# Optimization experiments

Hardware: AMD Instinct MI355X
Metric: run time of the kernel (lower is better)

## Reference

```python
import jax, jax.numpy as jnp
import numpy as np

B, H, KVH, D, CACHE = 16, 32, 8, 128, 4096


def _rope(x, cos, sin):
    # x: [B, S, Hx, D]; cos/sin: [B, S, 1, D//2] -- complex rotation on (even, odd) pairs
    xe, xo = x[..., ::2], x[..., 1::2]
    re = xe * cos - xo * sin
    im = xe * sin + xo * cos
    return jnp.stack([re, im], axis=-1).reshape(x.shape)


def setup_inputs() -> dict:
    key = jax.random.key(0)
    ks = jax.random.split(key, 8)
    xq = jax.random.normal(ks[0], (B, 1, H, D), jnp.float32)
    xk = jax.random.normal(ks[1], (B, 1, KVH, D), jnp.float32)
    xv = jax.random.normal(ks[2], (B, 1, KVH, D), jnp.float32)
    input_pos = jax.random.randint(ks[3], (B,), 1024, CACHE - 1, dtype=jnp.int32)
    inv_freq = 1.0 / (10000.0 ** (jnp.arange(0, D, 2, dtype=jnp.float32) / D))
    ang = input_pos.astype(jnp.float32)[:, None] * inv_freq[None, :]  # [B, D/2]
    freqs_cos = jnp.cos(ang)[:, None, :]  # [B, 1, D/2]
    freqs_sin = jnp.sin(ang)[:, None, :]
    cache_k = jax.random.randint(ks[4], (B, KVH, CACHE, D), -127, 128, dtype=jnp.int32)
    cache_v = jax.random.randint(ks[5], (B, KVH, CACHE, D), -127, 128, dtype=jnp.int32)
    k_scaler = jax.random.uniform(ks[6], (B, KVH, CACHE), jnp.float32, minval=0.005, maxval=0.05)
    v_scaler = jax.random.uniform(ks[7], (B, KVH, CACHE), jnp.float32, minval=0.005, maxval=0.05)
    return dict(xq=xq, xk=xk, xv=xv, freqs_cos=freqs_cos, freqs_sin=freqs_sin,
                k_scaler=k_scaler, v_scaler=v_scaler, cache_k=cache_k, cache_v=cache_v,
                input_pos=input_pos)


def reference(xq, xk, xv, freqs_cos, freqs_sin, k_scaler, v_scaler, cache_k, cache_v, input_pos):
    B_, S_, H_, D_ = xq.shape
    KVH_ = xk.shape[2]
    n_rep = H_ // KVH_
    cos, sin = freqs_cos[:, :, None, :], freqs_sin[:, :, None, :]
    q = _rope(xq, cos, sin)
    k = _rope(xk, cos, sin)
    # new decode token, [B, KVH, D]
    k_new = jnp.transpose(k, (0, 2, 1, 3))[:, :, 0, :]
    v_new = jnp.transpose(xv, (0, 2, 1, 3))[:, :, 0, :]
    # per-token, per-kv-head int8 quantization of the new K/V
    k_s = jnp.max(jnp.abs(k_new), axis=-1, keepdims=True) / 127.0 + 1e-8
    v_s = jnp.max(jnp.abs(v_new), axis=-1, keepdims=True) / 127.0 + 1e-8
    k_q = jnp.clip(jnp.round(k_new / k_s), -127, 127).astype(cache_k.dtype)
    v_q = jnp.clip(jnp.round(v_new / v_s), -127, 127).astype(cache_v.dtype)
    b_idx = jnp.arange(B_)
    cache_k = cache_k.at[b_idx, :, input_pos].set(k_q)
    cache_v = cache_v.at[b_idx, :, input_pos].set(v_q)
    k_scaler = k_scaler.at[b_idx, :, input_pos].set(k_s[..., 0])
    v_scaler = v_scaler.at[b_idx, :, input_pos].set(v_s[..., 0])
    # GQA: group query heads per kv head instead of materializing repeat_kv
    qg = jnp.transpose(q, (0, 2, 1, 3)).reshape(B_, KVH_, n_rep, D_)  # S_ == 1
    scores = jnp.einsum('bkrd,bksd->bkrs', qg, cache_k.astype(jnp.float32))
    scores = scores / jnp.sqrt(jnp.float32(D_)) * k_scaler[:, :, None, :]  # inline K dequant
    S_cache = cache_k.shape[2]
    mask = jnp.where(jnp.arange(S_cache)[None, :] <= input_pos[:, None], 0.0, -1e30)
    probs = jax.nn.softmax(scores + mask[:, None, None, :].astype(scores.dtype), axis=-1)
    out = jnp.einsum('bkrs,bksd->bkrd', probs * v_scaler[:, :, None, :], cache_v.astype(jnp.float32))
    return out.reshape(B_, H_, 1, D_)
```

## Files before the change

### kernel.cpp

```cpp
#include <hip/hip_runtime.h>
#include <hip/hip_bf16.h>
#include <cstdint>
#include <cstddef>

#define BATCH 16
#define HQ 32
#define KVHN 8
#define NREP 4
#define DIM 128
#define CACHE_LEN 4096
#define STATE_POS 128
#define NSTATE (CACHE_LEN / STATE_POS)

__global__ __launch_bounds__(64) void attn_partial(
    const float* __restrict__ xq,
    const float* __restrict__ fcos,
    const float* __restrict__ fsin,
    const float* __restrict__ k_scaler,
    const float* __restrict__ v_scaler,
    const int*   __restrict__ cache_k,
    const int*   __restrict__ cache_v,
    const int*   __restrict__ input_pos,
    float* __restrict__ ws_acc,
    float* __restrict__ ws_ml)
{
    const int state = blockIdx.x;
    const int kvh   = blockIdx.y;
    const int b     = blockIdx.z;
    const int pos   = input_pos[b];
    const int start = state * STATE_POS;
    if (start >= pos) return;

    const int lane = threadIdx.x;
    const int g    = lane >> 4;
    const int sl   = lane & 15;
    const int d0   = sl * 8;

    const int send = min(start + STATE_POS, pos);
    const float rsD = 0.088388347648318447f;

    float q[4][8];
    {
        float4 c4 = *(const float4*)(fcos + b * 64 + sl * 4);
        float4 s4 = *(const float4*)(fsin + b * 64 + sl * 4);
        c4.x *= rsD; c4.y *= rsD; c4.z *= rsD; c4.w *= rsD;
        s4.x *= rsD; s4.y *= rsD; s4.z *= rsD; s4.w *= rsD;
        #pragma unroll
        for (int r = 0; r < 4; ++r) {
            const float* qp = xq + ((size_t)(b * HQ + kvh * NREP + r)) * DIM + d0;
            const float4 x0 = *(const float4*)qp;
            const float4 x1 = *(const float4*)(qp + 4);
            q[r][0] = x0.x * c4.x - x0.y * s4.x;
            q[r][1] = x0.x * s4.x + x0.y * c4.x;
            q[r][2] = x0.z * c4.y - x0.w * s4.y;
            q[r][3] = x0.z * s4.y + x0.w * c4.y;
            q[r][4] = x1.x * c4.z - x1.y * s4.z;
            q[r][5] = x1.x * s4.z + x1.y * c4.z;
            q[r][6] = x1.z * c4.w - x1.w * s4.w;
            q[r][7] = x1.z * s4.w + x1.w * c4.w;
        }
    }

    const int bk = b * KVHN + kvh;
    const int*   __restrict__ kb = cache_k + (size_t)bk * CACHE_LEN * DIM;
    const int*   __restrict__ vb = cache_v + (size_t)bk * CACHE_LEN * DIM;
    const float* __restrict__ ks = k_scaler + (size_t)bk * CACHE_LEN;
    const float* __restrict__ vs = v_scaler + (size_t)bk * CACHE_LEN;

    __shared__ float4 ssc4[STATE_POS];

    float mloc[4] = {-1e30f, -1e30f, -1e30f, -1e30f};

    #pragma unroll 4
    for (int i = 0; i < STATE_POS / 4; ++i) {
        const int s = start + i * 4 + g;
        const int* kp = kb + (size_t)s * DIM + d0;
        const int4 kk0 = *(const int4*)kp;
        const int4 kk1 = *(const int4*)(kp + 4);
        const float k0 = (float)kk0.x, k1 = (float)kk0.y, k2 = (float)kk0.z, k3 = (float)kk0.w;
        const float k4 = (float)kk1.x, k5 = (float)kk1.y, k6 = (float)kk1.z, k7 = (float)kk1.w;
        float p[4];
        #pragma unroll
        for (int r = 0; r < 4; ++r) {
            p[r] = q[r][0] * k0 + q[r][1] * k1 + q[r][2] * k2 + q[r][3] * k3
                 + q[r][4] * k4 + q[r][5] * k5 + q[r][6] * k6 + q[r][7] * k7;
        }
        #pragma unroll
        for (int mask = 1; mask <= 8; mask <<= 1) {
            #pragma unroll
            for (int r = 0; r < 4; ++r) p[r] += __shfl_xor(p[r], mask, 64);
        }
        const float scale = ks[s];
        const bool valid = s < send;
        float4 sc;
        sc.x = valid ? p[0] * scale : -1e30f;
        sc.y = valid ? p[1] * scale : -1e30f;
        sc.z = valid ? p[2] * scale : -1e30f;
        sc.w = valid ? p[3] * scale : -1e30f;
        mloc[0] = fmaxf(mloc[0], sc.x);
        mloc[1] = fmaxf(mloc[1], sc.y);
        mloc[2] = fmaxf(mloc[2], sc.z);
        mloc[3] = fmaxf(mloc[3], sc.w);
        if (sl == 0) ssc4[i * 4 + g] = sc;
    }

    #pragma unroll
    for (int r = 0; r < 4; ++r) {
        mloc[r] = fmaxf(mloc[r], __shfl_xor(mloc[r], 16, 64));
        mloc[r] = fmaxf(mloc[r], __shfl_xor(mloc[r], 32, 64));
    }
    __syncthreads();

    float l[4] = {0.f, 0.f, 0.f, 0.f};
    float acc[4][8] = {};
    #pragma unroll 4
    for (int i = 0; i < STATE_POS / 4; ++i) {
        const int s = start + i * 4 + g;
        const int* vp = vb + (size_t)s * DIM + d0;
        const int4 vv0 = *(const int4*)vp;
        const int4 vv1 = *(const int4*)(vp + 4);
        const float vsc = vs[s];
        const float4 sc = ssc4[i * 4 + g];
        const float v0 = (float)vv0.x, v1 = (float)vv0.y, v2 = (float)vv0.z, v3 = (float)vv0.w;
        const float v4 = (float)vv1.x, v5 = (float)vv1.y, v6 = (float)vv1.z, v7 = (float)vv1.w;
        const float scr[4] = {sc.x, sc.y, sc.z, sc.w};
        #pragma unroll
        for (int r = 0; r < 4; ++r) {
            const float pr = __expf(scr[r] - mloc[r]);
            l[r] += pr;
            const float pv = pr * vsc;
            acc[r][0] += pv * v0; acc[r][1] += pv * v1;
            acc[r][2] += pv * v2; acc[r][3] += pv * v3;
            acc[r][4] += pv * v4; acc[r][5] += pv * v5;
            acc[r][6] += pv * v6; acc[r][7] += pv * v7;
        }
    }

    #pragma unroll
    for (int mask = 16; mask <= 32; mask <<= 1) {
        #pragma unroll
        for (int r = 0; r < 4; ++r) {
            l[r] += __shfl_xor(l[r], mask, 64);
            #pragma unroll
            for (int c = 0; c < 8; ++c) acc[r][c] += __shfl_xor(acc[r][c], mask, 64);
        }
    }

    if (g == 0) {
        float* abase = ws_acc + (((size_t)bk * NSTATE + state) * 4) * DIM;
        #pragma unroll
        for (int r = 0; r < 4; ++r) {
            float4 a0 = make_float4(acc[r][0], acc[r][1], acc[r][2], acc[r][3]);
            float4 a1 = make_float4(acc[r][4], acc[r][5], acc[r][6], acc[r][7]);
            *(float4*)(abase + r * DIM + d0)     = a0;
            *(float4*)(abase + r * DIM + d0 + 4) = a1;
        }
        if (sl == 0) {
            float* mlb = ws_ml + ((size_t)bk * NSTATE + state) * 8;
            #pragma unroll
            for (int r = 0; r < 4; ++r) { mlb[2 * r] = mloc[r]; mlb[2 * r + 1] = l[r]; }
        }
    }
}

__global__ __launch_bounds__(256) void attn_combine(
    const float* __restrict__ xq,
    const float* __restrict__ xk,
    const float* __restrict__ xv,
    const float* __restrict__ fcos,
    const float* __restrict__ fsin,
    const int*   __restrict__ input_pos,
    const float* __restrict__ ws_acc,
    const float* __restrict__ ws_ml,
    float* __restrict__ out)
{
    const int bk  = blockIdx.x;
    const int b   = bk >> 3;
    const int kvh = bk & 7;
    const int pos = input_pos[b];
    const int nst = min(NSTATE, (pos + STATE_POS - 1) / STATE_POS);

    const int t    = threadIdx.x;
    const int lane = t & 63;
    const int w    = t >> 6;

    __shared__ float sq[4][DIM];
    __shared__ float skq[DIM];
    __shared__ float svd[DIM];
    __shared__ float sml[NSTATE][8];
    __shared__ float ssc[4];
    __shared__ float sks, svs;

    const float rsD = 0.088388347648318447f;

    {
        const float c  = fcos[b * 64 + lane];
        const float s  = fsin[b * 64 + lane];
        const size_t qb = ((size_t)(b * HQ + kvh * NREP + w)) * DIM;
        const float xe = xq[qb + 2 * lane];
        const float xo = xq[qb + 2 * lane + 1];
        sq[w][2 * lane]     = xe * c - xo * s;
        sq[w][2 * lane + 1] = xe * s + xo * c;
    }
    if (w == 0) {
        const float c  = fcos[b * 64 + lane];
        const float s  = fsin[b * 64 + lane];
        const size_t kbb = ((size_t)(b * KVHN + kvh)) * DIM;
        const float xe = xk[kbb + 2 * lane];
        const float xo = xk[kbb + 2 * lane + 1];
        skq[2 * lane]     = xe * c - xo * s;
        skq[2 * lane + 1] = xe * s + xo * c;
    }
    if (t < nst * 8) sml[t >> 3][t & 7] = ws_ml[(size_t)bk * NSTATE * 8 + t];
    __syncthreads();

    if (w == 0) {
        float a = fmaxf(fabsf(skq[lane]), fabsf(skq[64 + lane]));
        #pragma unroll
        for (int mask = 32; mask; mask >>= 1) a = fmaxf(a, __shfl_xor(a, mask, 64));
        if (lane == 0) sks = a / 127.0f + 1e-8f;
    } else if (w == 1) {
        const size_t vbb = ((size_t)(b * KVHN + kvh)) * DIM;
        float a = fmaxf(fabsf(xv[vbb + lane]), fabsf(xv[vbb + 64 + lane]));
        #pragma unroll
        for (int mask = 32; mask; mask >>= 1) a = fmaxf(a, __shfl_xor(a, mask, 64));
        if (lane == 0) svs = a / 127.0f + 1e-8f;
    }
    __syncthreads();

    if (t < DIM) {
        skq[t] = fminf(fmaxf(rintf(skq[t] / sks), -127.f), 127.f);
    } else {
        const int d = t - DIM;
        const size_t vbb = ((size_t)(b * KVHN + kvh)) * DIM;
        const float vq = fminf(fmaxf(rintf(xv[vbb + d] / svs), -127.f), 127.f);
        svd[d] = vq * svs;
    }
    __syncthreads();

    {
        float sum = sq[w][lane] * skq[lane] + sq[w][64 + lane] * skq[64 + lane];
        #pragma unroll
        for (int mask = 32; mask; mask >>= 1) sum += __shfl_xor(sum, mask, 64);
        if (lane == 0) ssc[w] = sum * rsD * sks;
    }
    __syncthreads();

    const int r  = w;
    const int db = lane;
    float M = ssc[r];
    for (int s2 = 0; s2 < nst; ++s2) M = fmaxf(M, sml[s2][2 * r]);
    const float pn = __expf(ssc[r] - M);
    float L  = pn;
    float o0 = pn * svd[db];
    float o1 = pn * svd[db + 64];
    const float* ab = ws_acc + (size_t)bk * NSTATE * 4 * DIM;
    for (int s2 = 0; s2 < nst; ++s2) {
        const float al = __expf(sml[s2][2 * r] - M);
        L  += sml[s2][2 * r + 1] * al;
        o0 += ab[((size_t)(s2 * 4 + r)) * DIM + db]      * al;
        o1 += ab[((size_t)(s2 * 4 + r)) * DIM + db + 64] * al;
    }
    const float invL = 1.0f / L;
    float* ob = out + ((size_t)(b * HQ + kvh * NREP + r)) * DIM;
    ob[db]      = o0 * invL;
    ob[db + 64] = o1 * invL;
}

extern "C" void kernel_launch(void* const* d_in, const int* in_sizes, int n_in,
                              void* d_out, int out_size, void* d_ws, size_t ws_size,
                              hipStream_t stream)
{
    const float* xq        = (const float*)d_in[0];
    const float* xk        = (const float*)d_in[1];
    const float* xv        = (const float*)d_in[2];
    const float* fcos      = (const float*)d_in[3];
    const float* fsin      = (const float*)d_in[4];
    const float* k_scaler  = (const float*)d_in[5];
    const float* v_scaler  = (const float*)d_in[6];
    const int*   cache_k   = (const int*)d_in[7];
    const int*   cache_v   = (const int*)d_in[8];
    const int*   input_pos = (const int*)d_in[9];
    float* out = (float*)d_out;

    float* ws_acc = (float*)d_ws;
    float* ws_ml  = ws_acc + (size_t)BATCH * KVHN * NSTATE * 4 * DIM;

    dim3 g1(NSTATE, KVHN, BATCH);
    attn_partial<<<g1, 64, 0, stream>>>(xq, fcos, fsin, k_scaler, v_scaler,
                                        cache_k, cache_v, input_pos, ws_acc, ws_ml);
    attn_combine<<<BATCH * KVHN, 256, 0, stream>>>(xq, xk, xv, fcos, fsin,
                                                   input_pos, ws_acc, ws_ml, out);
}
```

Baseline: 503.7 us.

## Replace two-pass softmax with single pass using Cauchy-Schwarz max bound

Drops the separate max pass and the shared-memory score buffer in the partial kernel. Instead it computes an upper bound on each block's scores from the norm of q, the int8 range and the block's largest k scale, and exponentiates against that bound in one fused K/V pass. The state size is halved to 64 positions, which doubles the number of blocks and partials, and the combine loader now loops so it can read the larger partial count. The risk is underflow: if the bound sits far above the true max, exp values can vanish and precision is lost.

```diff
diff --git a/kernel.cpp b/kernel.cpp
--- a/kernel.cpp
+++ b/kernel.cpp
@@ -9,7 +9,7 @@
 #define NREP 4
 #define DIM 128
 #define CACHE_LEN 4096
-#define STATE_POS 128
+#define STATE_POS 64
 #define NSTATE (CACHE_LEN / STATE_POS)
 
 __global__ __launch_bounds__(64) void attn_partial(
@@ -39,6 +39,17 @@
     const int send = min(start + STATE_POS, pos);
     const float rsD = 0.088388347648318447f;
 
+    const int bk = b * KVHN + kvh;
+    const int*   __restrict__ kb = cache_k + (size_t)bk * CACHE_LEN * DIM;
+    const int*   __restrict__ vb = cache_v + (size_t)bk * CACHE_LEN * DIM;
+    const float* __restrict__ ks = k_scaler + (size_t)bk * CACHE_LEN;
+    const float* __restrict__ vs = v_scaler + (size_t)bk * CACHE_LEN;
+
+    float ksmax = ks[start + lane];
+    #pragma unroll
+    for (int mask = 32; mask; mask >>= 1)
+        ksmax = fmaxf(ksmax, __shfl_xor(ksmax, mask, 64));
+
     float q[4][8];
     {
         float4 c4 = *(const float4*)(fcos + b * 64 + sl * 4);
@@ -61,22 +72,32 @@
         }
     }
 
-    const int bk = b * KVHN + kvh;
-    const int*   __restrict__ kb = cache_k + (size_t)bk * CACHE_LEN * DIM;
-    const int*   __restrict__ vb = cache_v + (size_t)bk * CACHE_LEN * DIM;
-    const float* __restrict__ ks = k_scaler + (size_t)bk * CACHE_LEN;
-    const float* __restrict__ vs = v_scaler + (size_t)bk * CACHE_LEN;
-
-    __shared__ float4 ssc4[STATE_POS];
-
-    float mloc[4] = {-1e30f, -1e30f, -1e30f, -1e30f};
+    float M_ub[4];
+    #pragma unroll
+    for (int r = 0; r < 4; ++r) {
+        float nq = q[r][0]*q[r][0] + q[r][1]*q[r][1] + q[r][2]*q[r][2] + q[r][3]*q[r][3]
+                 + q[r][4]*q[r][4] + q[r][5]*q[r][5] + q[r][6]*q[r][6] + q[r][7]*q[r][7];
+        #pragma unroll
+        for (int mask = 1; mask <= 8; mask <<= 1) nq += __shfl_xor(nq, mask, 64);
+        M_ub[r] = sqrtf(nq) * 1436.8398f * ksmax;
+    }
+
+    float l[4] = {0.f, 0.f, 0.f, 0.f};
+    float acc[4][8] = {};
 
     #pragma unroll 4
     for (int i = 0; i < STATE_POS / 4; ++i) {
         const int s = start + i * 4 + g;
         const int* kp = kb + (size_t)s * DIM + d0;
+        const int* vp = vb + (size_t)s * DIM + d0;
         const int4 kk0 = *(const int4*)kp;
         const int4 kk1 = *(const int4*)(kp + 4);
+        const int4 vv0 = *(const int4*)vp;
+        const int4 vv1 = *(const int4*)(vp + 4);
+        const float scale = ks[s];
+        const float vsc   = vs[s];
+        const bool valid  = s < send;
+
         const float k0 = (float)kk0.x, k1 = (float)kk0.y, k2 = (float)kk0.z, k3 = (float)kk0.w;
         const float k4 = (float)kk1.x, k5 = (float)kk1.y, k6 = (float)kk1.z, k7 = (float)kk1.w;
         float p[4];
@@ -90,43 +111,12 @@
             #pragma unroll
             for (int r = 0; r < 4; ++r) p[r] += __shfl_xor(p[r], mask, 64);
         }
-        const float scale = ks[s];
-        const bool valid = s < send;
-        float4 sc;
-        sc.x = valid ? p[0] * scale : -1e30f;
-        sc.y = valid ? p[1] * scale : -1e30f;
-        sc.z = valid ? p[2] * scale : -1e30f;
-        sc.w = valid ? p[3] * scale : -1e30f;
-        mloc[0] = fmaxf(mloc[0], sc.x);
-        mloc[1] = fmaxf(mloc[1], sc.y);
-        mloc[2] = fmaxf(mloc[2], sc.z);
-        mloc[3] = fmaxf(mloc[3], sc.w);
-        if (sl == 0) ssc4[i * 4 + g] = sc;
-    }
-
-    #pragma unroll
-    for (int r = 0; r < 4; ++r) {
-        mloc[r] = fmaxf(mloc[r], __shfl_xor(mloc[r], 16, 64));
-        mloc[r] = fmaxf(mloc[r], __shfl_xor(mloc[r], 32, 64));
-    }
-    __syncthreads();
-
-    float l[4] = {0.f, 0.f, 0.f, 0.f};
-    float acc[4][8] = {};
-    #pragma unroll 4
-    for (int i = 0; i < STATE_POS / 4; ++i) {
-        const int s = start + i * 4 + g;
-        const int* vp = vb + (size_t)s * DIM + d0;
-        const int4 vv0 = *(const int4*)vp;
-        const int4 vv1 = *(const int4*)(vp + 4);
-        const float vsc = vs[s];
-        const float4 sc = ssc4[i * 4 + g];
+
         const float v0 = (float)vv0.x, v1 = (float)vv0.y, v2 = (float)vv0.z, v3 = (float)vv0.w;
         const float v4 = (float)vv1.x, v5 = (float)vv1.y, v6 = (float)vv1.z, v7 = (float)vv1.w;
-        const float scr[4] = {sc.x, sc.y, sc.z, sc.w};
-        #pragma unroll
-        for (int r = 0; r < 4; ++r) {
-            const float pr = __expf(scr[r] - mloc[r]);
+        #pragma unroll
+        for (int r = 0; r < 4; ++r) {
+            float pr = valid ? __expf(p[r] * scale - M_ub[r]) : 0.f;
             l[r] += pr;
             const float pv = pr * vsc;
             acc[r][0] += pv * v0; acc[r][1] += pv * v1;
@@ -158,7 +148,7 @@
         if (sl == 0) {
             float* mlb = ws_ml + ((size_t)bk * NSTATE + state) * 8;
             #pragma unroll
-            for (int r = 0; r < 4; ++r) { mlb[2 * r] = mloc[r]; mlb[2 * r + 1] = l[r]; }
+            for (int r = 0; r < 4; ++r) { mlb[2 * r] = M_ub[r]; mlb[2 * r + 1] = l[r]; }
         }
     }
 }
@@ -211,7 +201,8 @@
         skq[2 * lane]     = xe * c - xo * s;
         skq[2 * lane + 1] = xe * s + xo * c;
     }
-    if (t < nst * 8) sml[t >> 3][t & 7] = ws_ml[(size_t)bk * NSTATE * 8 + t];
+    for (int j = t; j < nst * 8; j += 256)
+        sml[j >> 3][j & 7] = ws_ml[(size_t)bk * NSTATE * 8 + j];
     __syncthreads();
 
     if (w == 0) {
```

New measurement: 518.4 us. +2.9%, slower.
